# Performance work log

Measured on AMD Instinct MI355X. Metric: run time of the kernel, lower is better.

## Reference

```python
import jax, jax.numpy as jnp
import numpy as np

B, D, K = 512, 128, 131072
TEMP = 0.07
PTR = 0  # queue_ptr starts at 0; B <= K so single contiguous write


def _normalize(x, axis):
    return x / jnp.linalg.norm(x, axis=axis, keepdims=True)


def setup_inputs() -> dict:
    key = jax.random.key(0)
    k = jax.random.split(key, 7)
    return {
        "predict0": jax.random.normal(k[0], (B, D), jnp.float32),
        "predict1": jax.random.normal(k[1], (B, D), jnp.float32),
        "project0": jax.random.normal(k[2], (B, D), jnp.float32),
        "project1": jax.random.normal(k[3], (B, D), jnp.float32),
        "queue": jax.random.normal(k[4], (D, K), jnp.float32),
        "queue_id": jax.random.randint(k[5], (K,), 0, 100000, jnp.int64) if jax.config.jax_enable_x64 else jax.random.randint(k[5], (K,), 0, 100000, jnp.int32),
        "ids": jax.random.randint(k[6], (B,), 0, 100000, jnp.int64) if jax.config.jax_enable_x64 else jax.random.randint(k[6], (B,), 0, 100000, jnp.int32),
    }


def _find_nn(proj, queue_n, queue_id, ids):
    # [B, K] similarity, mask out entries with same sample id, argmax, gather cols
    sim = proj @ queue_n                                   # [B, K]
    is_own = queue_id[None, :] == ids[:, None]             # [B, K]
    sim = jnp.where(is_own, jnp.float32(-1.0), sim)
    idx = jnp.argmax(sim, axis=1)                          # [B]
    return queue_n[:, idx]                                 # [D, B]


def _nnclr_loss(predicted, nn, temperature):
    # logits[i, j] = nn_i . predicted_j / T ; labels = arange(B)
    logits = (nn.T @ predicted.T) / temperature            # [B, B]
    logp = jax.nn.log_softmax(logits, axis=-1)
    return -jnp.mean(jnp.diagonal(logp))


def reference(predict0, predict1, project0, project1, queue, queue_id, ids):
    # forward_encoder's normalization (encoder itself is external and modeled out)
    p0 = _normalize(predict0, 1)
    p1 = _normalize(predict1, 1)
    z0 = _normalize(project0, 1)
    z1 = _normalize(project1, 1)
    queue_n = _normalize(queue, 0)  # queue stored normalized along dim 0

    # find_nn / queue are no_grad in the original
    nn0 = jax.lax.stop_gradient(_find_nn(jax.lax.stop_gradient(z0), queue_n, queue_id, ids))
    nn1 = jax.lax.stop_gradient(_find_nn(jax.lax.stop_gradient(z1), queue_n, queue_id, ids))

    loss0 = _nnclr_loss(p0, nn1, TEMP)
    loss1 = _nnclr_loss(p1, nn0, TEMP)
    loss = (loss0 + loss1) * 0.5

    # _dequeue_and_enqueue: ptr=0, B <= K -> contiguous slice write
    new_queue = jax.lax.dynamic_update_slice(queue_n, jax.lax.stop_gradient(z0.T), (0, PTR))
    new_queue_id = jax.lax.dynamic_update_slice(queue_id, ids, (PTR,))
    new_ptr = jnp.array((PTR + B) % K, dtype=queue_id.dtype)
    return loss, new_queue, new_queue_id, new_ptr
```

## Files before the change

### kernel.cpp

```cpp
#include <hip/hip_runtime.h>
#include <hip/hip_bf16.h>

typedef _Float16 half8 __attribute__((ext_vector_type(8)));
typedef _Float16 half4 __attribute__((ext_vector_type(4)));
typedef float f32x4 __attribute__((ext_vector_type(4)));

#define B 512
#define D 128
#define K 131072
#define TEMP 0.07f
#define NKB 256
#define KT_PER 32
#define NSS 16

#define INVN_OFF 0
#define Z0_OFF   131072
#define Z1_OFF   196608
#define P0_OFF   262144
#define P1_OFF   327680
#define ZF16_OFF 393216
#define QA_OFF   458752
#define PVAL_OFF 8847360
#define IDX_OFF  9373696
#define LP_OFF   9374720

__device__ __forceinline__ void gload_lds16(const _Float16* g, _Float16* l) {
  __builtin_amdgcn_global_load_lds(
      (const __attribute__((address_space(1))) unsigned int*)g,
      (__attribute__((address_space(3))) unsigned int*)l, 16, 0, 0);
}

__global__ __launch_bounds__(128) void rownorm_k(
    const float* __restrict__ p0, const float* __restrict__ p1,
    const float* __restrict__ z0, const float* __restrict__ z1,
    float* __restrict__ w, _Float16* __restrict__ zf16) {
  int row = blockIdx.x & (B - 1);
  int which = blockIdx.x >> 9;
  const float* src; float* dst;
  switch (which) {
    case 0: src = z0; dst = w + Z0_OFF; break;
    case 1: src = z1; dst = w + Z1_OFF; break;
    case 2: src = p0; dst = w + P0_OFF; break;
    default: src = p1; dst = w + P1_OFF; break;
  }
  int tid = threadIdx.x;
  float v = src[row * D + tid];
  float s = v * v;
  #pragma unroll
  for (int o = 32; o; o >>= 1) s += __shfl_xor(s, o);
  __shared__ float sm[2];
  if ((tid & 63) == 0) sm[tid >> 6] = s;
  __syncthreads();
  float inv = rsqrtf(sm[0] + sm[1]);
  float nv = v * inv;
  dst[row * D + tid] = nv;
  if (which < 2) zf16[(which * B + row) * D + tid] = (_Float16)nv;
}

__global__ __launch_bounds__(256) void colq_k(
    const float* __restrict__ q, const int* __restrict__ qid,
    const int* __restrict__ ids, const float* __restrict__ w_z0,
    float* __restrict__ invn, float* __restrict__ out,
    _Float16* __restrict__ qA) {
  __shared__ float psum[8][128];
  __shared__ float invs[128];
  __shared__ float sm2[2];
  __shared__ float fcol[128];
  __shared__ _Float16 tile[128][136];
  int tid = threadIdx.x;
  int kb = blockIdx.x;
  int k0 = kb * 128;
  int kc = tid & 31, dg = tid >> 5;

  float fqv = 0.f;
  if (kb > 4 && tid < 128) fqv = q[(size_t)tid * K + (k0 - 1)];

  float4 v[16];
  {
    float4 acc = {0.f, 0.f, 0.f, 0.f};
    #pragma unroll
    for (int i = 0; i < 16; i++) {
      int d = dg * 16 + i;
      v[i] = *(const float4*)(q + (size_t)d * K + k0 + kc * 4);
      acc.x = fmaf(v[i].x, v[i].x, acc.x); acc.y = fmaf(v[i].y, v[i].y, acc.y);
      acc.z = fmaf(v[i].z, v[i].z, acc.z); acc.w = fmaf(v[i].w, v[i].w, acc.w);
    }
    *(float4*)&psum[dg][kc * 4] = acc;
  }
  __syncthreads();
  if (tid < 128) {
    float s = 0.f;
    #pragma unroll
    for (int g2 = 0; g2 < 8; g2++) s += psum[g2][tid];
    float inv = rsqrtf(s);
    invs[tid] = inv;
    invn[k0 + tid] = inv;
    int kk = k0 + tid;
    out[1 + (size_t)D * K + kk] = (float)((kk < B) ? ids[kk] : qid[kk]);
  }
  if (kb > 4 && tid < 128) {
    float s2 = fqv * fqv;
    #pragma unroll
    for (int o = 32; o; o >>= 1) s2 += __shfl_xor(s2, o);
    if ((tid & 63) == 0) sm2[tid >> 6] = s2;
  }
  __syncthreads();
  if (kb > 4) {
    if (tid < 128) fcol[tid] = fqv * rsqrtf(sm2[0] + sm2[1]);
  } else if (kb == 4) {
    if (tid < 32)
      *(float4*)&fcol[tid * 4] = *(const float4*)(w_z0 + (size_t)511 * D + tid * 4);
  }
  __syncthreads();

  float4 iv = *(const float4*)&invs[kc * 4];
  if (kb >= 4) {
    #pragma unroll
    for (int i = 0; i < 16; i++) {
      int d = dg * 16 + i;
      float o0 = v[i].x * iv.x, o1 = v[i].y * iv.y;
      float o2 = v[i].z * iv.z, o3 = v[i].w * iv.w;
      half4 t = {(_Float16)o0, (_Float16)o1, (_Float16)o2, (_Float16)o3};
      *(half4*)&tile[d][kc * 4] = t;
      float p3 = __shfl_up(o3, 1);
      float x0 = (kc == 0) ? fcol[d] : p3;
      float4 st = {x0, o0, o1, o2};
      *(float4*)(out + (size_t)d * K + k0 + kc * 4) = st;
      if (kb == 1023 && kc == 31)
        out[1 + (size_t)d * K + (K - 1)] = o3;
    }
  } else {
    #pragma unroll
    for (int i = 0; i < 16; i++) {
      int d = dg * 16 + i;
      float o0 = v[i].x * iv.x, o1 = v[i].y * iv.y;
      float o2 = v[i].z * iv.z, o3 = v[i].w * iv.w;
      half4 t = {(_Float16)o0, (_Float16)o1, (_Float16)o2, (_Float16)o3};
      *(half4*)&tile[d][kc * 4] = t;
      float* oc = out + 1 + (size_t)d * K + k0 + kc * 4;
      int col = k0 + kc * 4;
      oc[0] = w_z0[(size_t)(col + 0) * D + d];
      oc[1] = w_z0[(size_t)(col + 1) * D + d];
      oc[2] = w_z0[(size_t)(col + 2) * D + d];
      oc[3] = w_z0[(size_t)(col + 3) * D + d];
    }
  }
  __syncthreads();
  {
    int dc = tid >> 6, l = tid & 63;
    int g = l >> 4, c = l & 15;
    #pragma unroll
    for (int kt = 0; kt < 8; kt++) {
      half8 f;
      #pragma unroll
      for (int i = 0; i < 8; i++) {
        int d = g * 4 + (i & 3) + ((i >> 2) << 4) + dc * 32;
        f[i] = tile[d][kt * 16 + c];
      }
      int ktg = kb * 8 + kt;
      *(half8*)(qA + (size_t)((ktg * 4 + dc) * 64 + l) * 8) = f;
    }
  }
}

#define PROCESS(AF, Q4) do { \
  _Pragma("unroll") \
  for (int nt = 0; nt < 4; nt++) { \
    f32x4 acc = {0.f, 0.f, 0.f, 0.f}; \
    _Pragma("unroll") \
    for (int dc = 0; dc < 4; dc++) \
      acc = __builtin_amdgcn_mfma_f32_16x16x32_f16(AF[dc], bf[nt][dc], acc, 0, 0, 0); \
    _Pragma("unroll") \
    for (int r = 0; r < 4; r++) { \
      int qv_ = (r == 0) ? Q4.x : (r == 1) ? Q4.y : (r == 2) ? Q4.z : Q4.w; \
      float sm_ = (qv_ == myid[nt]) ? -1.0f : acc[r]; \
      best[nt] = fmaxf(best[nt], sm_); \
    } \
  } \
} while (0)

__global__ __launch_bounds__(256) void nnsearch_k(
    const _Float16* __restrict__ qA, const _Float16* __restrict__ zf16,
    const int* __restrict__ qid, const int* __restrict__ ids,
    float* __restrict__ pval) {
  __shared__ __align__(16) _Float16 qtile[3][2][2048];
  __shared__ __align__(16) int qid_lds[512];
  int tid = threadIdx.x;
  int flat = blockIdx.x;
  int cls = flat & 7;
  int kb = cls * 32 + (flat >> 5);
  int rg = (flat >> 3) & 3;
  int wave = tid >> 6, lane = tid & 63;
  int g = lane >> 4, c = lane & 15;
  int rowbase = rg * 256 + wave * 64;
  int kt0 = kb * KT_PER;

  #pragma unroll
  for (int j = 0; j < 2; j++)
    gload_lds16(qA + (size_t)(((kt0 + j) * 4 + wave) * 64 + lane) * 8,
                &qtile[0][j][wave * 512]);
  #pragma unroll
  for (int j = 0; j < 2; j++)
    gload_lds16(qA + (size_t)(((kt0 + 2 + j) * 4 + wave) * 64 + lane) * 8,
                &qtile[1][j][wave * 512]);
  qid_lds[tid] = qid[kb * 512 + tid];
  qid_lds[tid + 256] = qid[kb * 512 + tid + 256];

  half8 bf[4][4];
  int myid[4];
  #pragma unroll
  for (int nt = 0; nt < 4; nt++) {
    int row = rowbase + nt * 16 + c;
    myid[nt] = ids[row & (B - 1)];
    #pragma unroll
    for (int dc = 0; dc < 4; dc++) {
      const _Float16* zr = zf16 + row * D + dc * 32 + g * 4;
      half4 lo = *(const half4*)zr;
      half4 hi = *(const half4*)(zr + 16);
      half8 f = {lo[0], lo[1], lo[2], lo[3], hi[0], hi[1], hi[2], hi[3]};
      bf[nt][dc] = f;
    }
  }
  __syncthreads();

  float best[4] = {-2.f, -2.f, -2.f, -2.f};
  int cur = 0;
  for (int s = 0; s < NSS; s++) {
    half8 af0[4], af1[4];
    #pragma unroll
    for (int dc = 0; dc < 4; dc++)
      af0[dc] = *(const half8*)&qtile[cur][0][dc * 512 + lane * 8];
    #pragma unroll
    for (int dc = 0; dc < 4; dc++)
      af1[dc] = *(const half8*)&qtile[cur][1][dc * 512 + lane * 8];
    int4 q4a = *(const int4*)&qid_lds[(s * 2 + 0) * 16 + g * 4];
    int4 q4b = *(const int4*)&qid_lds[(s * 2 + 1) * 16 + g * 4];
    if (s + 2 < NSS) {
      int nbuf = cur + 2; if (nbuf >= 3) nbuf -= 3;
      #pragma unroll
      for (int j = 0; j < 2; j++)
        gload_lds16(qA + (size_t)(((kt0 + (s + 2) * 2 + j) * 4 + wave) * 64 + lane) * 8,
                    &qtile[nbuf][j][wave * 512]);
    }
    PROCESS(af0, q4a);
    PROCESS(af1, q4b);
    if (s < NSS - 1) {
      asm volatile("s_waitcnt lgkmcnt(0)" ::: "memory");
      if (s + 2 < NSS) asm volatile("s_waitcnt vmcnt(2)" ::: "memory");
      else             asm volatile("s_waitcnt vmcnt(0)" ::: "memory");
      __builtin_amdgcn_sched_barrier(0);
      __builtin_amdgcn_s_barrier();
      __builtin_amdgcn_sched_barrier(0);
    }
    cur += 1; if (cur >= 3) cur -= 3;
  }

  #pragma unroll
  for (int nt = 0; nt < 4; nt++) {
    float v = best[nt];
    v = fmaxf(v, __shfl_xor(v, 16));
    v = fmaxf(v, __shfl_xor(v, 32));
    if (g == 0) {
      int row = rowbase + nt * 16 + c;
      pval[row * NKB + kb] = v;
    }
  }
}

__global__ __launch_bounds__(256) void nnpick_k(
    const float* __restrict__ pval, const _Float16* __restrict__ qA,
    const _Float16* __restrict__ zf16, const int* __restrict__ qid,
    const int* __restrict__ ids, int* __restrict__ idxout) {
  int row = blockIdx.x;
  int tid = threadIdx.x;
  int wave = tid >> 6, lane = tid & 63;
  int g = lane >> 4;
  __shared__ unsigned sv[4];
  __shared__ unsigned skb[4];
  __shared__ int s_kb;
  __shared__ float s_wv;
  {
    float a = pval[row * NKB + tid];
    unsigned v = (__float_as_uint(fmaf(a, 0.5f, 3.0f)) << 9) | (unsigned)(NKB - 1 - tid);
    #pragma unroll
    for (int o = 32; o; o >>= 1) {
      unsigned ov = __shfl_xor(v, o);
      v = v > ov ? v : ov;
    }
    if (lane == 0) sv[wave] = v;
  }
  __syncthreads();
  if (tid == 0) {
    unsigned v = sv[0];
    #pragma unroll
    for (int wv = 1; wv < 4; wv++) v = v > sv[wv] ? v : sv[wv];
    int kbw = (NKB - 1) - (int)(v & 0x1FFu);
    s_kb = kbw;
    s_wv = pval[row * NKB + kbw];
  }
  __syncthreads();
  int kb = s_kb;
  float wv = s_wv;
  int myid = ids[row & (B - 1)];

  half8 bf[4];
  #pragma unroll
  for (int dc = 0; dc < 4; dc++) {
    const _Float16* zr = zf16 + row * D + dc * 32 + g * 4;
    half4 lo = *(const half4*)zr;
    half4 hi = *(const half4*)(zr + 16);
    half8 f = {lo[0], lo[1], lo[2], lo[3], hi[0], hi[1], hi[2], hi[3]};
    bf[dc] = f;
  }

  unsigned kbest = 0x7FFFFFFFu;
  int ktbase = kb * KT_PER + wave * 8;
  for (int kt = 0; kt < 8; kt++) {
    int ktg = ktbase + kt;
    half8 af[4];
    #pragma unroll
    for (int dc = 0; dc < 4; dc++)
      af[dc] = *(const half8*)(qA + (size_t)((ktg * 4 + dc) * 64 + lane) * 8);
    int4 q4 = *(const int4*)(qid + ktg * 16 + g * 4);
    f32x4 acc = {0.f, 0.f, 0.f, 0.f};
    #pragma unroll
    for (int dc = 0; dc < 4; dc++)
      acc = __builtin_amdgcn_mfma_f32_16x16x32_f16(af[dc], bf[dc], acc, 0, 0, 0);
    #pragma unroll
    for (int r = 0; r < 4; r++) {
      int qv = (r == 0) ? q4.x : (r == 1) ? q4.y : (r == 2) ? q4.z : q4.w;
      float sm = (qv == myid) ? -1.0f : acc[r];
      if (sm == wv) {
        unsigned kk = (unsigned)(ktg * 16 + g * 4 + r);
        kbest = kbest < kk ? kbest : kk;
      }
    }
  }
  unsigned o1 = __shfl_xor(kbest, 16); kbest = kbest < o1 ? kbest : o1;
  unsigned o2 = __shfl_xor(kbest, 32); kbest = kbest < o2 ? kbest : o2;
  if (lane == 0) skb[wave] = kbest;
  __syncthreads();
  if (tid == 0) {
    unsigned v = skb[0];
    #pragma unroll
    for (int wv2 = 1; wv2 < 4; wv2++) v = v < skb[wv2] ? v : skb[wv2];
    idxout[row] = (int)(v < (K - 1) ? v : (K - 1));
  }
}

__global__ __launch_bounds__(256) void loss_k(
    const float* __restrict__ q, const float* __restrict__ invn,
    const int* __restrict__ idxout, const float* __restrict__ w,
    float* __restrict__ lpart) {
  int i0 = blockIdx.x * 8;
  int v = blockIdx.y;
  int tid = threadIdx.x;
  __shared__ float nns[8][D];
  __shared__ float rm[8][4], re[8][4], sdlds[8];
  #pragma unroll
  for (int ii = 0; ii < 4; ii++) {
    int i = ii * 2 + (tid >> 7);
    int d = tid & 127;
    int nnidx = idxout[(v ? 0 : B) + i0 + i];
    nns[i][d] = q[(size_t)d * K + nnidx] * invn[nnidx];
  }
  __syncthreads();
  const float* pr = w + (v ? P1_OFF : P0_OFF);
  const float* r0 = pr + tid * D;
  const float* r1 = pr + (tid + 256) * D;
  float a0[8] = {0, 0, 0, 0, 0, 0, 0, 0};
  float a1[8] = {0, 0, 0, 0, 0, 0, 0, 0};
  for (int d = 0; d < D; d += 4) {
    float4 x0 = *(const float4*)(r0 + d);
    float4 x1 = *(const float4*)(r1 + d);
    #pragma unroll
    for (int i = 0; i < 8; i++) {
      float4 n = *(const float4*)&nns[i][d];
      a0[i] = fmaf(x0.x, n.x, a0[i]); a0[i] = fmaf(x0.y, n.y, a0[i]);
      a0[i] = fmaf(x0.z, n.z, a0[i]); a0[i] = fmaf(x0.w, n.w, a0[i]);
      a1[i] = fmaf(x1.x, n.x, a1[i]); a1[i] = fmaf(x1.y, n.y, a1[i]);
      a1[i] = fmaf(x1.z, n.z, a1[i]); a1[i] = fmaf(x1.w, n.w, a1[i]);
    }
  }
  #pragma unroll
  for (int i = 0; i < 8; i++) {
    a0[i] *= (1.0f / TEMP);
    a1[i] *= (1.0f / TEMP);
  }
  #pragma unroll
  for (int i = 0; i < 8; i++) {
    int ig = i0 + i;
    if ((ig & 256) == 0) { if (tid == ig) sdlds[i] = a0[i]; }
    else { if (tid == (ig & 255)) sdlds[i] = a1[i]; }
  }
  int wv = tid >> 6;
  #pragma unroll
  for (int i = 0; i < 8; i++) {
    float m = fmaxf(a0[i], a1[i]);
    #pragma unroll
    for (int o = 32; o; o >>= 1) m = fmaxf(m, __shfl_xor(m, o));
    if ((tid & 63) == 0) rm[i][wv] = m;
  }
  __syncthreads();
  #pragma unroll
  for (int i = 0; i < 8; i++) {
    float m = fmaxf(fmaxf(rm[i][0], rm[i][1]), fmaxf(rm[i][2], rm[i][3]));
    float e = expf(a0[i] - m) + expf(a1[i] - m);
    #pragma unroll
    for (int o = 32; o; o >>= 1) e += __shfl_xor(e, o);
    if ((tid & 63) == 0) re[i][wv] = e;
  }
  __syncthreads();
  if (tid < 8) {
    int i = tid;
    float m = fmaxf(fmaxf(rm[i][0], rm[i][1]), fmaxf(rm[i][2], rm[i][3]));
    float s = re[i][0] + re[i][1] + re[i][2] + re[i][3];
    lpart[v * B + i0 + i] = sdlds[i] - m - logf(s);
  }
}

__global__ __launch_bounds__(256) void final_k(
    const float* __restrict__ lpart, float* __restrict__ out) {
  int tid = threadIdx.x;
  float s = lpart[tid] + lpart[tid + 256] + lpart[tid + 512] + lpart[tid + 768];
  #pragma unroll
  for (int o = 32; o; o >>= 1) s += __shfl_xor(s, o);
  __shared__ float sm[4];
  if ((tid & 63) == 0) sm[tid >> 6] = s;
  __syncthreads();
  if (tid == 0) {
    float total = sm[0] + sm[1] + sm[2] + sm[3];
    out[0] = -total * (1.0f / 1024.0f);
    out[1 + D * K + K] = 512.0f;
  }
}

extern "C" void kernel_launch(void* const* d_in, const int* in_sizes, int n_in,
                              void* d_out, int out_size, void* d_ws, size_t ws_size,
                              hipStream_t stream) {
  const float* p0 = (const float*)d_in[0];
  const float* p1 = (const float*)d_in[1];
  const float* z0 = (const float*)d_in[2];
  const float* z1 = (const float*)d_in[3];
  const float* q  = (const float*)d_in[4];
  const int* qid  = (const int*)d_in[5];
  const int* ids  = (const int*)d_in[6];
  float* out = (float*)d_out;
  float* w = (float*)d_ws;
  float* invn = w + INVN_OFF;
  _Float16* zf16 = (_Float16*)(w + ZF16_OFF);
  _Float16* qA   = (_Float16*)(w + QA_OFF);
  float* pval = w + PVAL_OFF;
  int* idxout = (int*)(w + IDX_OFF);
  float* lpart = w + LP_OFF;

  rownorm_k<<<2048, 128, 0, stream>>>(p0, p1, z0, z1, w, zf16);
  colq_k<<<K / 128, 256, 0, stream>>>(q, qid, ids, w + Z0_OFF, invn, out, qA);
  nnsearch_k<<<1024, 256, 0, stream>>>(qA, zf16, qid, ids, pval);
  nnpick_k<<<1024, 256, 0, stream>>>(pval, qA, zf16, qid, ids, idxout);
  dim3 gl(B / 8, 2);
  loss_k<<<gl, 256, 0, stream>>>(q, invn, idxout, w, lpart);
  final_k<<<1, 256, 0, stream>>>(lpart, out);
}
```

Measured before the change: 113.9 us.

## Precompute per-tile id-match mask to skip masking in NN search

Adds a kernel that flags, for each group of 16 queue entries, whether any queue id matches any batch id, and stores this as a 16-bit mask. The NN search kernel reads the mask per tile and, when no match exists, takes a clean path that max-reduces the MFMA accumulators without per-element id comparisons. It also raises wave priority around the MFMA section. The cost is an extra kernel launch doing a 512-way compare for every queue entry.

```diff
diff --git a/kernel.cpp b/kernel.cpp
--- a/kernel.cpp
+++ b/kernel.cpp
@@ -23,6 +23,7 @@
 #define PVAL_OFF 8847360
 #define IDX_OFF  9373696
 #define LP_OFF   9374720
+#define IDM_OFF  9375744
 
 __device__ __forceinline__ void gload_lds16(const _Float16* g, _Float16* l) {
   __builtin_amdgcn_global_load_lds(
@@ -55,6 +56,28 @@
   float nv = v * inv;
   dst[row * D + tid] = nv;
   if (which < 2) zf16[(which * B + row) * D + tid] = (_Float16)nv;
+}
+
+__global__ __launch_bounds__(256) void idmask_k(
+    const int* __restrict__ qid, const int* __restrict__ ids,
+    unsigned short* __restrict__ idm) {
+  __shared__ int sids[B];
+  int tid = threadIdx.x;
+  sids[tid] = ids[tid];
+  sids[tid + 256] = ids[tid + 256];
+  __syncthreads();
+  int k = blockIdx.x * 256 + tid;
+  int myq = qid[k];
+  bool match = false;
+  #pragma unroll 4
+  for (int j = 0; j < B; j += 4) {
+    int4 i4 = *(const int4*)&sids[j];
+    match |= (myq == i4.x) | (myq == i4.y) | (myq == i4.z) | (myq == i4.w);
+  }
+  unsigned long long bal = __ballot(match);
+  int lane = tid & 63;
+  if ((lane & 15) == 0)
+    idm[k >> 4] = (unsigned short)((bal >> lane) & 0xFFFFull);
 }
 
 __global__ __launch_bounds__(256) void colq_k(
@@ -179,12 +202,25 @@
   } \
 } while (0)
 
+#define PROCESS_CLEAN(AF) do { \
+  _Pragma("unroll") \
+  for (int nt = 0; nt < 4; nt++) { \
+    f32x4 acc = {0.f, 0.f, 0.f, 0.f}; \
+    _Pragma("unroll") \
+    for (int dc = 0; dc < 4; dc++) \
+      acc = __builtin_amdgcn_mfma_f32_16x16x32_f16(AF[dc], bf[nt][dc], acc, 0, 0, 0); \
+    best[nt] = fmaxf(best[nt], \
+        fmaxf(fmaxf(acc[0], acc[1]), fmaxf(acc[2], acc[3]))); \
+  } \
+} while (0)
+
 __global__ __launch_bounds__(256) void nnsearch_k(
     const _Float16* __restrict__ qA, const _Float16* __restrict__ zf16,
     const int* __restrict__ qid, const int* __restrict__ ids,
-    float* __restrict__ pval) {
+    const unsigned short* __restrict__ idm, float* __restrict__ pval) {
   __shared__ __align__(16) _Float16 qtile[3][2][2048];
   __shared__ __align__(16) int qid_lds[512];
+  __shared__ unsigned short qmask_lds[32];
   int tid = threadIdx.x;
   int flat = blockIdx.x;
   int cls = flat & 7;
@@ -205,6 +241,7 @@
                 &qtile[1][j][wave * 512]);
   qid_lds[tid] = qid[kb * 512 + tid];
   qid_lds[tid + 256] = qid[kb * 512 + tid + 256];
+  if (tid < 32) qmask_lds[tid] = idm[kt0 + tid];
 
   half8 bf[4][4];
   int myid[4];
@@ -233,8 +270,8 @@
     #pragma unroll
     for (int dc = 0; dc < 4; dc++)
       af1[dc] = *(const half8*)&qtile[cur][1][dc * 512 + lane * 8];
-    int4 q4a = *(const int4*)&qid_lds[(s * 2 + 0) * 16 + g * 4];
-    int4 q4b = *(const int4*)&qid_lds[(s * 2 + 1) * 16 + g * 4];
+    int ma = qmask_lds[s * 2 + 0];
+    int mb = qmask_lds[s * 2 + 1];
     if (s + 2 < NSS) {
       int nbuf = cur + 2; if (nbuf >= 3) nbuf -= 3;
       #pragma unroll
@@ -242,8 +279,20 @@
         gload_lds16(qA + (size_t)(((kt0 + (s + 2) * 2 + j) * 4 + wave) * 64 + lane) * 8,
                     &qtile[nbuf][j][wave * 512]);
     }
-    PROCESS(af0, q4a);
-    PROCESS(af1, q4b);
+    __builtin_amdgcn_s_setprio(1);
+    if (ma) {
+      int4 q4a = *(const int4*)&qid_lds[(s * 2 + 0) * 16 + g * 4];
+      PROCESS(af0, q4a);
+    } else {
+      PROCESS_CLEAN(af0);
+    }
+    if (mb) {
+      int4 q4b = *(const int4*)&qid_lds[(s * 2 + 1) * 16 + g * 4];
+      PROCESS(af1, q4b);
+    } else {
+      PROCESS_CLEAN(af1);
+    }
+    __builtin_amdgcn_s_setprio(0);
     if (s < NSS - 1) {
       asm volatile("s_waitcnt lgkmcnt(0)" ::: "memory");
       if (s + 2 < NSS) asm volatile("s_waitcnt vmcnt(2)" ::: "memory");
@@ -453,10 +502,12 @@
   float* pval = w + PVAL_OFF;
   int* idxout = (int*)(w + IDX_OFF);
   float* lpart = w + LP_OFF;
+  unsigned short* idm = (unsigned short*)(w + IDM_OFF);
 
   rownorm_k<<<2048, 128, 0, stream>>>(p0, p1, z0, z1, w, zf16);
+  idmask_k<<<K / 256, 256, 0, stream>>>(qid, ids, idm);
   colq_k<<<K / 128, 256, 0, stream>>>(q, qid, ids, w + Z0_OFF, invn, out, qA);
-  nnsearch_k<<<1024, 256, 0, stream>>>(qA, zf16, qid, ids, pval);
+  nnsearch_k<<<1024, 256, 0, stream>>>(qA, zf16, qid, ids, idm, pval);
   nnpick_k<<<1024, 256, 0, stream>>>(pval, qA, zf16, qid, ids, idxout);
   dim3 gl(B / 8, 2);
   loss_k<<<gl, 256, 0, stream>>>(q, invn, idxout, w, lpart);
```

Result: slower. 120.2 us, median of 2 (+5.6%).
